# Kernel optimization log

Measured on AMD Instinct MI355X. Metric: run time of the kernel, lower is better.

Reference implementation:

```python
import jax, jax.numpy as jnp
import numpy as np

D_MODEL = 1024
N_SA = 8          # self-attention heads
N_RA = 8          # relational-attention heads
TOTAL = N_SA + N_RA
HEAD_DIM = D_MODEL // TOTAL   # 64
KEY_DIM = HEAD_DIM            # default key_dim = d_model // total_n_heads
N_REL = 8                     # n_relations (= n_heads_ra default)
REL_PROJ = KEY_DIM            # rel_proj_dim default
B, S = 4, 1024


def _rope(x, cos, sin):
    # x: [b, s, h, d]; cos/sin: [s, d//2]; interleaved-pair rotation as in apply_rotary_emb
    xr = x.reshape(x.shape[:-1] + (-1, 2))
    x_r, x_i = xr[..., 0], xr[..., 1]
    c = cos[None, :, None, :]
    s = sin[None, :, None, :]
    o_r = x_r * c - x_i * s
    o_i = x_r * s + x_i * c
    return jnp.stack([o_r, o_i], axis=-1).reshape(x.shape)


def setup_inputs() -> dict:
    key = jax.random.key(0)
    ks = jax.random.split(key, 16)
    def p(k, shape, scale=0.02):
        return jax.random.normal(k, shape, dtype=jnp.float32) * scale
    x = jax.random.normal(ks[0], (B, S, D_MODEL), dtype=jnp.float32)
    symbols = jax.random.normal(ks[1], (B, S, D_MODEL), dtype=jnp.float32)
    # standard RoPE frequency tables, shape [S, KEY_DIM//2]
    inv_freq = 1.0 / (10000.0 ** (np.arange(0, KEY_DIM, 2, dtype=np.float32) / KEY_DIM))
    ang = np.outer(np.arange(S, dtype=np.float32), inv_freq)
    freqs_cos = jnp.asarray(np.cos(ang), dtype=jnp.float32)
    freqs_sin = jnp.asarray(np.sin(ang), dtype=jnp.float32)
    return dict(
        x=x, symbols=symbols, freqs_cos=freqs_cos, freqs_sin=freqs_sin,
        # self-attention stream params
        wq_sa=p(ks[2], (D_MODEL, N_SA * KEY_DIM)),
        wk_sa=p(ks[3], (D_MODEL, N_SA * KEY_DIM)),
        wv_sa=p(ks[4], (D_MODEL, N_SA * HEAD_DIM)),
        wo_sa=p(ks[5], (N_SA * HEAD_DIM, N_SA * HEAD_DIM)),
        # relational-attention stream params
        wq_attn=p(ks[6], (D_MODEL, N_RA * KEY_DIM)),
        wk_attn=p(ks[7], (D_MODEL, N_RA * KEY_DIM)),
        wq_rel=p(ks[8], (D_MODEL, N_REL * REL_PROJ)),
        wk_rel=p(ks[9], (D_MODEL, N_REL * REL_PROJ)),
        wr=p(ks[10], (N_RA, HEAD_DIM, N_REL)),      # per-head relation->head_dim map
        wv_sym=p(ks[11], (D_MODEL, N_RA * HEAD_DIM)),  # symbol projection
        wo_ra=p(ks[12], (N_RA * HEAD_DIM, N_RA * HEAD_DIM)),
    )


def reference(x, symbols, freqs_cos, freqs_sin, wq_sa, wk_sa, wv_sa, wo_sa,
              wq_attn, wk_attn, wq_rel, wk_rel, wr, wv_sym, wo_ra):
    b, s, _ = x.shape
    attn_scale = 1.0 / jnp.sqrt(jnp.asarray(HEAD_DIM, dtype=x.dtype))
    rel_scale = 1.0 / jnp.sqrt(jnp.asarray(REL_PROJ, dtype=x.dtype))
    causal = jnp.tril(jnp.ones((s, s), dtype=bool))
    neg = jnp.where(causal, jnp.asarray(0.0, x.dtype), jnp.asarray(-jnp.inf, x.dtype))

    # ---- standard self-attention stream ----
    q = _rope((x @ wq_sa).reshape(b, s, N_SA, KEY_DIM), freqs_cos, freqs_sin)
    k = _rope((x @ wk_sa).reshape(b, s, N_SA, KEY_DIM), freqs_cos, freqs_sin)
    v = (x @ wv_sa).reshape(b, s, N_SA, HEAD_DIM)
    scores = jnp.einsum('bihd,bjhd->bhij', q, k) * attn_scale + neg
    attn = jax.nn.softmax(scores, axis=-1)
    sa_out = jnp.einsum('bhij,bjhd->bihd', attn, v).reshape(b, s, -1) @ wo_sa

    # ---- relational attention stream ----
    qa = _rope((x @ wq_attn).reshape(b, s, N_RA, KEY_DIM), freqs_cos, freqs_sin)
    ka = _rope((x @ wk_attn).reshape(b, s, N_RA, KEY_DIM), freqs_cos, freqs_sin)
    ra_scores = jnp.einsum('bihd,bjhd->bhij', qa, ka) * attn_scale + neg
    ra_attn = jax.nn.softmax(ra_scores, axis=-1)
    # relations r(i,j) in R^{n_rel}: inner products of relation projections, tanh-activated
    qr = (x @ wq_rel).reshape(b, s, N_REL, REL_PROJ)
    kr = (x @ wk_rel).reshape(b, s, N_REL, REL_PROJ)
    rel = jnp.tanh(jnp.einsum('bird,bjrd->bijr', qr, kr) * rel_scale)  # [b,s,s,n_rel]
    sv = (symbols @ wv_sym).reshape(b, s, N_RA, HEAD_DIM)
    sym_msg = jnp.einsum('bhij,bjhd->bihd', ra_attn, sv)
    rel_msg = jnp.einsum('bhij,bijr->bihr', ra_attn, rel)
    rel_proj = jnp.einsum('bihr,hdr->bihd', rel_msg, wr)
    ra_out = (sym_msg + rel_proj).reshape(b, s, -1) @ wo_ra

    # dual attention: concat the two streams along feature dim -> [b, s, d_model]
    return jnp.concatenate([sa_out, ra_out], axis=-1)
```

## Files before the change

kernel.cpp:

```cpp
#include <hip/hip_runtime.h>

typedef unsigned short u16;
typedef unsigned int u32;
typedef __attribute__((ext_vector_type(8))) short s16x8;
typedef __attribute__((ext_vector_type(4))) float f32x4;

#define C_QSA 0
#define C_KSA 512
#define C_VSA 1024
#define C_QA  1536
#define C_KA  2048
#define C_QR  2560
#define C_KR  3072
#define C_SV  3584
#define LDP   4096

__device__ __forceinline__ u16 f2bf(float f) {
    union { float f; unsigned u; } v; v.f = f;
    return (u16)((v.u + 0x7FFFu + ((v.u >> 16) & 1u)) >> 16);
}
__device__ __forceinline__ float bf2f(u16 h) {
    union { unsigned u; float f; } v; v.u = ((unsigned)h) << 16; return v.f;
}
__device__ __forceinline__ float fexp(float y) {
    return __builtin_exp2f(y * 1.4426950408889634f);
}
__device__ __forceinline__ float ftanh(float x) {
    float e = __builtin_exp2f(x * 2.885390081777927f);
    return 1.f - 2.f / (e + 1.f);
}
__device__ __forceinline__ f32x4 mfma16(s16x8 a, s16x8 b, f32x4 c) {
    return __builtin_amdgcn_mfma_f32_16x16x32_bf16(a, b, c, 0, 0, 0);
}
__device__ __forceinline__ void gload16(const u16* g, u16* l) {
    __builtin_amdgcn_global_load_lds(
        (const __attribute__((address_space(1))) void*)g,
        (__attribute__((address_space(3))) void*)l, 16, 0, 0);
}


__global__ void cvt2_f32_bf16(const float* __restrict__ a, const float* __restrict__ b,
                              u16* __restrict__ oa, u16* __restrict__ ob) {
    int i = (blockIdx.x * 256 + threadIdx.x) * 8;
    const int half = (i >= 4194304) ? 1 : 0;
    const float* in = half ? b : a;
    u16* out = half ? ob : oa;
    int off = i - half * 4194304;
    float4 x = *(const float4*)(in + off);
    float4 y = *(const float4*)(in + off + 4);
    s16x8 o;
    o[0] = (short)f2bf(x.x); o[1] = (short)f2bf(x.y);
    o[2] = (short)f2bf(x.z); o[3] = (short)f2bf(x.w);
    o[4] = (short)f2bf(y.x); o[5] = (short)f2bf(y.y);
    o[6] = (short)f2bf(y.z); o[7] = (short)f2bf(y.w);
    *(s16x8*)(out + off) = o;
}

struct WP { const float* p[10]; };

__global__ void transpose_w(WP wp, u16* __restrict__ WcatT,
                            u16* __restrict__ woSaT, u16* __restrict__ woRaT) {
    const int z = blockIdx.z;
    const float* W;
    u16* Wt;
    int K;
    if (z < 8) { W = wp.p[z]; Wt = WcatT + (size_t)z * 524288; K = 1024; }
    else       { W = wp.p[z]; Wt = (z == 8) ? woSaT : woRaT;   K = 512;  }
    const int N = 512;
    const int kt = blockIdx.x * 32, nt = blockIdx.y * 32;
    if (kt >= K) return;
    __shared__ float t[32][33];
    const int c = threadIdx.x & 31, r0 = threadIdx.x >> 5;
#pragma unroll
    for (int it = 0; it < 4; ++it) {
        int r = it * 8 + r0;
        t[r][c] = W[(size_t)(kt + r) * N + nt + c];
    }
    __syncthreads();
#pragma unroll
    for (int it = 0; it < 4; ++it) {
        int r = it * 8 + r0;
        Wt[(size_t)(nt + r) * K + kt + c] = f2bf(t[c][r]);
    }
}

__global__ void transpose_v2(const u16* __restrict__ P, u16* __restrict__ Vt, int colOff) {
    const int st = blockIdx.x * 32, ht = blockIdx.y * 32, b = blockIdx.z;
    __shared__ u16 t[32][34];
    const int c = threadIdx.x & 31, r0 = threadIdx.x >> 5;
#pragma unroll
    for (int it = 0; it < 4; ++it) {
        int r = it * 8 + r0;
        t[r][c] = P[(size_t)(b * 1024 + st + r) * LDP + colOff + ht + c];
    }
    __syncthreads();
    const int cp = ((c & 15) >> 2) * 8 + (c >> 4) * 4 + (c & 3);
#pragma unroll
    for (int it = 0; it < 4; ++it) {
        int r = it * 8 + r0;
        Vt[(size_t)b * 524288 + (size_t)(ht + r) * 1024 + st + cp] = t[c][r];
    }
}


__global__ void rope_kernel(u16* __restrict__ P, const float* __restrict__ fcos,
                            const float* __restrict__ fsin) {
    int idx = blockIdx.x * 256 + threadIdx.x;
    int row = idx >> 10;
    int rem = idx & 1023;
    int region = rem >> 8;
    int pr = rem & 255;
    int head = pr >> 5, p = pr & 31;
    int off = (region + (region >> 1)) * 512;
    int col = off + head * 64 + 2 * p;
    int s = row & 1023;
    float c = fcos[s * 32 + p], sn = fsin[s * 32 + p];
    u32* ptr = (u32*)(P + (size_t)row * LDP + col);
    u32 v = *ptr;
    float xr = bf2f((u16)(v & 0xffff)), xi = bf2f((u16)(v >> 16));
    u16 o0 = f2bf(xr * c - xi * sn);
    u16 o1 = f2bf(xr * sn + xi * c);
    *ptr = (u32)o0 | ((u32)o1 << 16);
}


template<bool OUT_BF16, bool SWZ>
__global__ __launch_bounds__(256) void gemm_bf16(
    const u16* __restrict__ A, const u16* __restrict__ A2, int lda, int nswitch,
    const u16* __restrict__ Bt, int ldb,
    void* __restrict__ Cp, int ldc, int ccolOff, int K)
{
    __shared__ u16 As[128][64];
    __shared__ u16 Bs[128][64];
    const int tid = threadIdx.x;
    int bx = blockIdx.x, by = blockIdx.y;
    if (SWZ) {
        int lin = by * gridDim.x + bx;
        int k = lin & 7, j = lin >> 3;
        bx = (k & 3) * 8 + (j & 7);
        by = (k >> 2) * 16 + (j >> 3);
    }
    const int m0 = bx * 128, n0 = by * 128;
    const u16* Ause = (A2 != nullptr && n0 >= nswitch) ? A2 : A;
    const int w = tid >> 6, lane = tid & 63;
    const int w32 = w * 32;
    const int wm = (w >> 1) * 64, wn = (w & 1) * 64;
    const int lr = lane & 15, lg = lane >> 4;
    const int srow = lane >> 3;
    const int sc16 = ((lane & 7) ^ srow) * 8;
    f32x4 acc[4][4] = {};

    for (int k0 = 0; k0 < K; k0 += 64) {
        const u16* ga = &Ause[(size_t)(m0 + w32 + srow) * lda + k0 + sc16];
        const u16* gb = &Bt [(size_t)(n0 + w32 + srow) * ldb + k0 + sc16];
        gload16(ga,            &As[w32][0]);
        gload16(ga +  8 * lda, &As[w32 +  8][0]);
        gload16(ga + 16 * lda, &As[w32 + 16][0]);
        gload16(ga + 24 * lda, &As[w32 + 24][0]);
        gload16(gb,            &Bs[w32][0]);
        gload16(gb +  8 * ldb, &Bs[w32 +  8][0]);
        gload16(gb + 16 * ldb, &Bs[w32 + 16][0]);
        gload16(gb + 24 * ldb, &Bs[w32 + 24][0]);
        __syncthreads();
#pragma unroll
        for (int kk = 0; kk < 2; ++kk) {
            s16x8 af[4], bfr[4];
#pragma unroll
            for (int t = 0; t < 4; ++t) {
                const int ca = (((kk * 4 + lg) ^ (lr & 7)) * 8);
                af[t]  = *(const s16x8*)&As[wm + t * 16 + lr][ca];
                bfr[t] = *(const s16x8*)&Bs[wn + t * 16 + lr][ca];
            }
#pragma unroll
            for (int i = 0; i < 4; ++i)
#pragma unroll
                for (int j = 0; j < 4; ++j)
                    acc[i][j] = mfma16(af[i], bfr[j], acc[i][j]);
        }
        __syncthreads();
    }
#pragma unroll
    for (int i = 0; i < 4; ++i)
#pragma unroll
        for (int j = 0; j < 4; ++j)
#pragma unroll
            for (int r = 0; r < 4; ++r) {
                int row = m0 + wm + i * 16 + lg * 4 + r;
                int col = n0 + wn + j * 16 + lr;
                float val = acc[i][j][r];
                if (OUT_BF16)
                    ((u16*)Cp)[(size_t)row * ldc + ccolOff + col] = f2bf(val);
                else
                    ((float*)Cp)[(size_t)row * ldc + ccolOff + col] = val;
            }
}


__global__ __launch_bounds__(64) void attn_sa(u16* __restrict__ P, const u16* __restrict__ Vt) {
    const int bid = blockIdx.x;
    const int h = bid & 7;
    const int b = (bid >> 3) & 3;
    const int pr = bid >> 5;
    const int xt1 = pr, xt2 = 63 - pr;
    const int lane = threadIdx.x, lr = lane & 15, lg = lane >> 4;
    const size_t rowBase = (size_t)b * 1024;
    const int i0_1 = xt1 * 16, i0_2 = xt2 * 16;
    const int ir1 = i0_1 + lr, ir2 = i0_2 + lr;

    const u16* Kbase = P + rowBase * LDP + (C_KSA + h * 64);
    const u16* Vb = Vt + ((size_t)(b * 8 + h)) * 65536;

    s16x8 q1[2], q2[2];
    {
        const u16* q = P + (rowBase + ir1) * LDP + (C_QSA + h * 64) + lg * 8;
        q1[0] = *(const s16x8*)q; q1[1] = *(const s16x8*)(q + 32);
        q = P + (rowBase + ir2) * LDP + (C_QSA + h * 64) + lg * 8;
        q2[0] = *(const s16x8*)q; q2[1] = *(const s16x8*)(q + 32);
    }
    f32x4 o1[4] = {}, o2[4] = {};
    float l1 = 0.f, l2 = 0.f;
    const int njt  = (xt2 >> 1) + 1;
    const int njt1 = (xt1 >> 1) + 1;

    for (int jt = 0; jt < njt; ++jt) {
        const int j0 = jt * 32;
        const bool act1 = (jt < njt1);
        s16x8 kf[2][2], vfr[4];
#pragma unroll
        for (int sub = 0; sub < 2; ++sub) {
            const u16* kp = Kbase + (size_t)(j0 + sub * 16 + lr) * LDP + lg * 8;
            kf[sub][0] = *(const s16x8*)kp;
            kf[sub][1] = *(const s16x8*)(kp + 32);
        }
#pragma unroll
        for (int ds = 0; ds < 4; ++ds)
            vfr[ds] = *(const s16x8*)(Vb + (size_t)(ds * 16 + lr) * 1024 + j0 + 8 * lg);

        f32x4 sc2[2] = {{0.f,0.f,0.f,0.f},{0.f,0.f,0.f,0.f}};
        f32x4 sc1[2] = {{0.f,0.f,0.f,0.f},{0.f,0.f,0.f,0.f}};
#pragma unroll
        for (int sub = 0; sub < 2; ++sub) {
            sc2[sub] = mfma16(kf[sub][0], q2[0], sc2[sub]);
            sc2[sub] = mfma16(kf[sub][1], q2[1], sc2[sub]);
        }
        if (act1) {
#pragma unroll
            for (int sub = 0; sub < 2; ++sub) {
                sc1[sub] = mfma16(kf[sub][0], q1[0], sc1[sub]);
                sc1[sub] = mfma16(kf[sub][1], q1[1], sc1[sub]);
            }
        }
        s16x8 pa;
#pragma unroll
        for (int sub = 0; sub < 2; ++sub)
#pragma unroll
            for (int r = 0; r < 4; ++r) {
                int j = j0 + sub * 16 + 4 * lg + r;
                float p = (j <= ir2) ? fexp(sc2[sub][r] * 0.125f) : 0.f;
                l2 += p;
                pa[sub * 4 + r] = (short)f2bf(p);
            }
#pragma unroll
        for (int ds = 0; ds < 4; ++ds) o2[ds] = mfma16(pa, vfr[ds], o2[ds]);
        if (act1) {
#pragma unroll
            for (int sub = 0; sub < 2; ++sub)
#pragma unroll
                for (int r = 0; r < 4; ++r) {
                    int j = j0 + sub * 16 + 4 * lg + r;
                    float p = (j <= ir1) ? fexp(sc1[sub][r] * 0.125f) : 0.f;
                    l1 += p;
                    pa[sub * 4 + r] = (short)f2bf(p);
                }
#pragma unroll
            for (int ds = 0; ds < 4; ++ds) o1[ds] = mfma16(pa, vfr[ds], o1[ds]);
        }
    }
    l1 += __shfl_xor(l1, 16); l1 += __shfl_xor(l1, 32);
    l2 += __shfl_xor(l2, 16); l2 += __shfl_xor(l2, 32);
    float li1[4], li2[4];
#pragma unroll
    for (int r = 0; r < 4; ++r) {
        li1[r] = 1.f / __shfl(l1, 4 * lg + r);
        li2[r] = 1.f / __shfl(l2, 4 * lg + r);
    }
#pragma unroll
    for (int ds = 0; ds < 4; ++ds)
#pragma unroll
        for (int r = 0; r < 4; ++r) {
            P[(rowBase + i0_1 + 4 * lg + r) * LDP + (C_QSA + h * 64) + ds * 16 + lr] =
                f2bf(o1[ds][r] * li1[r]);
            P[(rowBase + i0_2 + 4 * lg + r) * LDP + (C_QSA + h * 64) + ds * 16 + lr] =
                f2bf(o2[ds][r] * li2[r]);
        }
}


__global__ __launch_bounds__(512) void attn_ra(u16* __restrict__ P, const u16* __restrict__ SVt,
                                               float* __restrict__ opart,
                                               float* __restrict__ mlr) {
    const int bid = blockIdx.x;
    const int slot = bid & 7;
    const int b = slot & 3, s = slot >> 2;
    const int xt = 63 - (bid >> 3);
    const int w = threadIdx.x >> 6, lane = threadIdx.x & 63;
    const int lr = lane & 15, lg = lane >> 4;
    const int h = w;
    const size_t rowBase = (size_t)b * 1024;
    const int i0 = xt * 16;
    const int ir = i0 + lr;

    __shared__ float relT[2][2][32][16][8];

    const u16* Kbase  = P + rowBase * LDP + (C_KA + h * 64);
    const u16* KRbase = P + rowBase * LDP + (C_KR + h * 64);
    const u16* Vb = SVt + ((size_t)(b * 8 + h)) * 65536;

    s16x8 qf[2], qrf[2];
    {
        const u16* q = P + (rowBase + ir) * LDP + (C_QA + h * 64) + lg * 8;
        qf[0] = *(const s16x8*)q; qf[1] = *(const s16x8*)(q + 32);
        const u16* qr = P + (rowBase + ir) * LDP + (C_QR + h * 64) + lg * 8;
        qrf[0] = *(const s16x8*)qr; qrf[1] = *(const s16x8*)(qr + 32);
    }
    f32x4 o[4] = {};
    float rmr[8] = {};
    float l = 0.f;
    const int njt = (xt >> 1) + 1;
    const int cnt = (njt - s + 1) >> 1;
    const int npair = (cnt + 1) >> 1;
    const int slotw = (w + lr) & 7;

    for (int u = 0; u < npair; ++u) {
        const int j0a = (s + 4 * u) * 32;
        const bool actB = (2 * u + 1) < cnt;
        const int j0b = actB ? j0a + 64 : j0a;
        s16x8 kfA[2][2], krA[2][2], kfB[2][2], krB[2][2], vfA[4], vfB[4];
#pragma unroll
        for (int sub = 0; sub < 2; ++sub) {
            const u16* kp = Kbase + (size_t)(j0a + sub * 16 + lr) * LDP + lg * 8;
            kfA[sub][0] = *(const s16x8*)kp;  kfA[sub][1] = *(const s16x8*)(kp + 32);
            const u16* krp = KRbase + (size_t)(j0a + sub * 16 + lr) * LDP + lg * 8;
            krA[sub][0] = *(const s16x8*)krp; krA[sub][1] = *(const s16x8*)(krp + 32);
            kp = Kbase + (size_t)(j0b + sub * 16 + lr) * LDP + lg * 8;
            kfB[sub][0] = *(const s16x8*)kp;  kfB[sub][1] = *(const s16x8*)(kp + 32);
            krp = KRbase + (size_t)(j0b + sub * 16 + lr) * LDP + lg * 8;
            krB[sub][0] = *(const s16x8*)krp; krB[sub][1] = *(const s16x8*)(krp + 32);
        }
#pragma unroll
        for (int ds = 0; ds < 4; ++ds) {
            vfA[ds] = *(const s16x8*)(Vb + (size_t)(ds * 16 + lr) * 1024 + j0a + 8 * lg);
            vfB[ds] = *(const s16x8*)(Vb + (size_t)(ds * 16 + lr) * 1024 + j0b + 8 * lg);
        }
        f32x4 scA[2] = {{0.f,0.f,0.f,0.f},{0.f,0.f,0.f,0.f}};
        f32x4 scB[2] = {{0.f,0.f,0.f,0.f},{0.f,0.f,0.f,0.f}};
        f32x4 rtA[2] = {{0.f,0.f,0.f,0.f},{0.f,0.f,0.f,0.f}};
        f32x4 rtB[2] = {{0.f,0.f,0.f,0.f},{0.f,0.f,0.f,0.f}};
#pragma unroll
        for (int sub = 0; sub < 2; ++sub) {
            scA[sub] = mfma16(kfA[sub][0], qf[0], scA[sub]);
            scA[sub] = mfma16(kfA[sub][1], qf[1], scA[sub]);
            rtA[sub] = mfma16(krA[sub][0], qrf[0], rtA[sub]);
            rtA[sub] = mfma16(krA[sub][1], qrf[1], rtA[sub]);
            scB[sub] = mfma16(kfB[sub][0], qf[0], scB[sub]);
            scB[sub] = mfma16(kfB[sub][1], qf[1], scB[sub]);
            rtB[sub] = mfma16(krB[sub][0], qrf[0], rtB[sub]);
            rtB[sub] = mfma16(krB[sub][1], qrf[1], rtB[sub]);
        }
        float pA[2][4], pB[2][4];
#pragma unroll
        for (int sub = 0; sub < 2; ++sub)
#pragma unroll
            for (int r = 0; r < 4; ++r) {
                int jA = j0a + sub * 16 + 4 * lg + r;
                int jB = j0b + sub * 16 + 4 * lg + r;
                pA[sub][r] = (jA <= ir) ? fexp(scA[sub][r] * 0.125f) : 0.f;
                pB[sub][r] = (actB && jB <= ir) ? fexp(scB[sub][r] * 0.125f) : 0.f;
                l += pA[sub][r] + pB[sub][r];
            }
#pragma unroll
        for (int sub = 0; sub < 2; ++sub)
#pragma unroll
            for (int r = 0; r < 4; ++r) {
                int jp = sub * 16 + 4 * lg + r;
                relT[u & 1][0][jp][lr][slotw] = ftanh(rtA[sub][r] * 0.125f);
                relT[u & 1][1][jp][lr][slotw] = ftanh(rtB[sub][r] * 0.125f);
            }
        __syncthreads();
#pragma unroll
        for (int sub = 0; sub < 2; ++sub)
#pragma unroll
            for (int r = 0; r < 4; ++r) {
                int jp = sub * 16 + 4 * lg + r;
                f32x4 a  = *(const f32x4*)&relT[u & 1][0][jp][lr][0];
                f32x4 bb = *(const f32x4*)&relT[u & 1][0][jp][lr][4];
                float pv = pA[sub][r];
#pragma unroll
                for (int k = 0; k < 4; ++k) {
                    rmr[k]     += pv * a[k];
                    rmr[4 + k] += pv * bb[k];
                }
                a  = *(const f32x4*)&relT[u & 1][1][jp][lr][0];
                bb = *(const f32x4*)&relT[u & 1][1][jp][lr][4];
                pv = pB[sub][r];
#pragma unroll
                for (int k = 0; k < 4; ++k) {
                    rmr[k]     += pv * a[k];
                    rmr[4 + k] += pv * bb[k];
                }
            }
        s16x8 paA, paB;
#pragma unroll
        for (int r = 0; r < 4; ++r) {
            paA[r]     = (short)f2bf(pA[0][r]);
            paA[4 + r] = (short)f2bf(pA[1][r]);
            paB[r]     = (short)f2bf(pB[0][r]);
            paB[4 + r] = (short)f2bf(pB[1][r]);
        }
#pragma unroll
        for (int ds = 0; ds < 4; ++ds) {
            o[ds] = mfma16(paA, vfA[ds], o[ds]);
            o[ds] = mfma16(paB, vfB[ds], o[ds]);
        }
    }

    l += __shfl_xor(l, 16); l += __shfl_xor(l, 32);
#pragma unroll
    for (int k = 0; k < 8; ++k) {
        float v = rmr[k];
        v += __shfl_xor(v, 16);
        v += __shfl_xor(v, 32);
        rmr[k] = v;
    }
    float g[8], t0[8];
    const int t = lr & 7;
#pragma unroll
    for (int k = 0; k < 8; ++k) g[k] = rmr[k];
#pragma unroll
    for (int k = 0; k < 8; ++k) t0[k] = (t & 1) ? g[(k + 1) & 7] : g[k];
#pragma unroll
    for (int k = 0; k < 8; ++k) g[k]  = (t & 2) ? t0[(k + 2) & 7] : t0[k];
#pragma unroll
    for (int k = 0; k < 8; ++k) t0[k] = (t & 4) ? g[(k + 4) & 7] : g[k];

    const int headRow = (b * 8 + h) * 1024;
#pragma unroll
    for (int ds = 0; ds < 4; ++ds)
#pragma unroll
        for (int r = 0; r < 4; ++r) {
            int row = headRow + i0 + 4 * lg + r;
            opart[((size_t)row * 2 + s) * 64 + ds * 16 + lr] = o[ds][r];
        }
    if (lg == 0) {
        float* pm = &mlr[((size_t)(headRow + i0 + lr) * 2 + s) * 10];
        pm[0] = l;
#pragma unroll
        for (int c = 0; c < 8; ++c) pm[1 + c] = t0[c];
    }
}


__global__ __launch_bounds__(256) void merge_ra(const float* __restrict__ opart,
                                                const float* __restrict__ mlr,
                                                const float* __restrict__ wr,
                                                u16* __restrict__ P) {
    const int gid = blockIdx.x * 4 + (threadIdx.x >> 6);
    const int d = threadIdx.x & 63;
    const int i = gid & 1023;
    const int h = (gid >> 10) & 7;
    const int b = gid >> 13;
    const float* ml0 = &mlr[(size_t)gid * 20];
    const float* ml1 = ml0 + 10;
    float ilt = 1.f / (ml0[0] + ml1[0]);
    float acc = (opart[(size_t)gid * 128 + d] +
                 opart[(size_t)gid * 128 + 64 + d]) * ilt;
#pragma unroll
    for (int c = 0; c < 8; ++c) {
        float rm = (ml0[1 + c] + ml1[1 + c]) * ilt;
        acc += rm * wr[h * 512 + d * 8 + c];
    }
    P[((size_t)(b * 1024 + i)) * LDP + C_QA + h * 64 + d] = f2bf(acc);
}


extern "C" void kernel_launch(void* const* d_in, const int* in_sizes, int n_in,
                              void* d_out, int out_size, void* d_ws, size_t ws_size,
                              hipStream_t stream)
{
    const float* x     = (const float*)d_in[0];
    const float* sym   = (const float*)d_in[1];
    const float* fcos  = (const float*)d_in[2];
    const float* fsin  = (const float*)d_in[3];
    const float* w_qsa = (const float*)d_in[4];
    const float* w_ksa = (const float*)d_in[5];
    const float* w_vsa = (const float*)d_in[6];
    const float* w_osa = (const float*)d_in[7];
    const float* w_qa  = (const float*)d_in[8];
    const float* w_ka  = (const float*)d_in[9];
    const float* w_qr  = (const float*)d_in[10];
    const float* w_kr  = (const float*)d_in[11];
    const float* wr    = (const float*)d_in[12];
    const float* w_sv  = (const float*)d_in[13];
    const float* w_ora = (const float*)d_in[14];

    char* ws = (char*)d_ws;
    u16* xb    = (u16*)(ws);
    u16* symb  = (u16*)(ws + (8u  << 20));
    u16* WcatT = (u16*)(ws + (16u << 20));
    u16* woSaT = (u16*)(ws + (24u << 20));
    u16* woRaT = (u16*)(ws + (24u << 20) + (512u << 10));
    u16* Pcat  = (u16*)(ws + (25u << 20));
    u16* vT    = (u16*)(ws + (57u << 20));
    u16* svT   = (u16*)(ws + (61u << 20));
    float* opart = (float*)(ws);
    float* mlrp  = (float*)(ws + (17u << 20));

    cvt2_f32_bf16<<<4096, 256, 0, stream>>>(x, sym, xb, symb);

    WP wp{{w_qsa, w_ksa, w_vsa, w_qa, w_ka, w_qr, w_kr, w_sv, w_osa, w_ora}};
    transpose_w<<<dim3(32, 16, 10), 256, 0, stream>>>(wp, WcatT, woSaT, woRaT);

    gemm_bf16<true, true><<<dim3(32, 32), 256, 0, stream>>>(
        xb, symb, 1024, C_SV, WcatT, 1024, Pcat, LDP, 0, 1024);

    rope_kernel<<<16384, 256, 0, stream>>>(Pcat, fcos, fsin);

    transpose_v2<<<dim3(32, 16, 4), 256, 0, stream>>>(Pcat, vT,  C_VSA);
    transpose_v2<<<dim3(32, 16, 4), 256, 0, stream>>>(Pcat, svT, C_SV);

    attn_sa<<<1024, 64, 0, stream>>>(Pcat, vT);
    attn_ra<<<512, 512, 0, stream>>>(Pcat, svT, opart, mlrp);
    merge_ra<<<8192, 256, 0, stream>>>(opart, mlrp, wr, Pcat);

    gemm_bf16<false, false><<<dim3(32, 8), 256, 0, stream>>>(
        Pcat + C_QSA, Pcat + C_QA, LDP, 512, woSaT, 512, d_out, 1024, 0, 512);
}
```

Measured before the change: 202.5 us.

## Fuse self-attention and relational-attention kernels into one interleaved launch

Merges the separate self-attention and relational-attention kernels into a single 768-block launch in which every third block row does self-attention (8 waves, one per head, on a 16-row tile) and the rest do relational attention. The aim is to remove a launch boundary and let the cheaper self-attention work fill gaps beside the heavier relational blocks. The self-attention path drops its earlier pairing of short and long causal tiles in favour of per-head waves with descending tile order. The relational path now uses a single-buffered shared relation tile with an extra barrier per iteration, which adds synchronisation in exchange for half the shared memory.

```diff
diff --git a/kernel.cpp b/kernel.cpp
--- a/kernel.cpp
+++ b/kernel.cpp
@@ -196,121 +196,91 @@
 }
 
 
-__global__ __launch_bounds__(64) void attn_sa(u16* __restrict__ P, const u16* __restrict__ Vt) {
+__global__ __launch_bounds__(512) void attn_fused(
+    u16* __restrict__ P, const u16* __restrict__ Vt, const u16* __restrict__ SVt,
+    float* __restrict__ opart, float* __restrict__ mlr)
+{
+    __shared__ float relT[2][32][16][8];
     const int bid = blockIdx.x;
-    const int h = bid & 7;
-    const int b = (bid >> 3) & 3;
-    const int pr = bid >> 5;
-    const int xt1 = pr, xt2 = 63 - pr;
-    const int lane = threadIdx.x, lr = lane & 15, lg = lane >> 4;
-    const size_t rowBase = (size_t)b * 1024;
-    const int i0_1 = xt1 * 16, i0_2 = xt2 * 16;
-    const int ir1 = i0_1 + lr, ir2 = i0_2 + lr;
-
-    const u16* Kbase = P + rowBase * LDP + (C_KSA + h * 64);
-    const u16* Vb = Vt + ((size_t)(b * 8 + h)) * 65536;
-
-    s16x8 q1[2], q2[2];
-    {
-        const u16* q = P + (rowBase + ir1) * LDP + (C_QSA + h * 64) + lg * 8;
-        q1[0] = *(const s16x8*)q; q1[1] = *(const s16x8*)(q + 32);
-        q = P + (rowBase + ir2) * LDP + (C_QSA + h * 64) + lg * 8;
-        q2[0] = *(const s16x8*)q; q2[1] = *(const s16x8*)(q + 32);
-    }
-    f32x4 o1[4] = {}, o2[4] = {};
-    float l1 = 0.f, l2 = 0.f;
-    const int njt  = (xt2 >> 1) + 1;
-    const int njt1 = (xt1 >> 1) + 1;
-
-    for (int jt = 0; jt < njt; ++jt) {
-        const int j0 = jt * 32;
-        const bool act1 = (jt < njt1);
-        s16x8 kf[2][2], vfr[4];
-#pragma unroll
-        for (int sub = 0; sub < 2; ++sub) {
-            const u16* kp = Kbase + (size_t)(j0 + sub * 16 + lr) * LDP + lg * 8;
-            kf[sub][0] = *(const s16x8*)kp;
-            kf[sub][1] = *(const s16x8*)(kp + 32);
-        }
-#pragma unroll
-        for (int ds = 0; ds < 4; ++ds)
-            vfr[ds] = *(const s16x8*)(Vb + (size_t)(ds * 16 + lr) * 1024 + j0 + 8 * lg);
-
-        f32x4 sc2[2] = {{0.f,0.f,0.f,0.f},{0.f,0.f,0.f,0.f}};
-        f32x4 sc1[2] = {{0.f,0.f,0.f,0.f},{0.f,0.f,0.f,0.f}};
-#pragma unroll
-        for (int sub = 0; sub < 2; ++sub) {
-            sc2[sub] = mfma16(kf[sub][0], q2[0], sc2[sub]);
-            sc2[sub] = mfma16(kf[sub][1], q2[1], sc2[sub]);
-        }
-        if (act1) {
-#pragma unroll
-            for (int sub = 0; sub < 2; ++sub) {
-                sc1[sub] = mfma16(kf[sub][0], q1[0], sc1[sub]);
-                sc1[sub] = mfma16(kf[sub][1], q1[1], sc1[sub]);
-            }
-        }
-        s16x8 pa;
-#pragma unroll
-        for (int sub = 0; sub < 2; ++sub)
-#pragma unroll
-            for (int r = 0; r < 4; ++r) {
-                int j = j0 + sub * 16 + 4 * lg + r;
-                float p = (j <= ir2) ? fexp(sc2[sub][r] * 0.125f) : 0.f;
-                l2 += p;
-                pa[sub * 4 + r] = (short)f2bf(p);
-            }
-#pragma unroll
-        for (int ds = 0; ds < 4; ++ds) o2[ds] = mfma16(pa, vfr[ds], o2[ds]);
-        if (act1) {
-#pragma unroll
-            for (int sub = 0; sub < 2; ++sub)
-#pragma unroll
-                for (int r = 0; r < 4; ++r) {
-                    int j = j0 + sub * 16 + 4 * lg + r;
-                    float p = (j <= ir1) ? fexp(sc1[sub][r] * 0.125f) : 0.f;
-                    l1 += p;
-                    pa[sub * 4 + r] = (short)f2bf(p);
-                }
-#pragma unroll
-            for (int ds = 0; ds < 4; ++ds) o1[ds] = mfma16(pa, vfr[ds], o1[ds]);
-        }
-    }
-    l1 += __shfl_xor(l1, 16); l1 += __shfl_xor(l1, 32);
-    l2 += __shfl_xor(l2, 16); l2 += __shfl_xor(l2, 32);
-    float li1[4], li2[4];
-#pragma unroll
-    for (int r = 0; r < 4; ++r) {
-        li1[r] = 1.f / __shfl(l1, 4 * lg + r);
-        li2[r] = 1.f / __shfl(l2, 4 * lg + r);
-    }
-#pragma unroll
-    for (int ds = 0; ds < 4; ++ds)
-#pragma unroll
-        for (int r = 0; r < 4; ++r) {
-            P[(rowBase + i0_1 + 4 * lg + r) * LDP + (C_QSA + h * 64) + ds * 16 + lr] =
-                f2bf(o1[ds][r] * li1[r]);
-            P[(rowBase + i0_2 + 4 * lg + r) * LDP + (C_QSA + h * 64) + ds * 16 + lr] =
-                f2bf(o2[ds][r] * li2[r]);
-        }
-}
-
-
-__global__ __launch_bounds__(512) void attn_ra(u16* __restrict__ P, const u16* __restrict__ SVt,
-                                               float* __restrict__ opart,
-                                               float* __restrict__ mlr) {
-    const int bid = blockIdx.x;
-    const int slot = bid & 7;
-    const int b = slot & 3, s = slot >> 2;
-    const int xt = 63 - (bid >> 3);
+    const int r = bid >> 3, xcd = bid & 7;
     const int w = threadIdx.x >> 6, lane = threadIdx.x & 63;
     const int lr = lane & 15, lg = lane >> 4;
+    const int rm3 = r % 3;
+
+    if (rm3 == 2) {
+        const int sa_blk = (r / 3) * 8 + xcd;
+        const int h = w;
+        const int b = sa_blk & 3;
+        const int xt = 63 - (sa_blk >> 2);
+        const size_t rowBase = (size_t)b * 1024;
+        const int i0 = xt * 16;
+        const int ir = i0 + lr;
+        const u16* Kbase = P + rowBase * LDP + (C_KSA + h * 64);
+        const u16* Vb = Vt + ((size_t)(b * 8 + h)) * 65536;
+
+        s16x8 qf[2];
+        {
+            const u16* q = P + (rowBase + ir) * LDP + (C_QSA + h * 64) + lg * 8;
+            qf[0] = *(const s16x8*)q;
+            qf[1] = *(const s16x8*)(q + 32);
+        }
+        f32x4 o[4] = {};
+        float l = 0.f;
+        const int njt = (xt >> 1) + 1;
+
+        for (int jt = 0; jt < njt; ++jt) {
+            const int j0 = jt * 32;
+            s16x8 kf[2][2], vfr[4];
+#pragma unroll
+            for (int sub = 0; sub < 2; ++sub) {
+                const u16* kp = Kbase + (size_t)(j0 + sub * 16 + lr) * LDP + lg * 8;
+                kf[sub][0] = *(const s16x8*)kp;
+                kf[sub][1] = *(const s16x8*)(kp + 32);
+            }
+#pragma unroll
+            for (int ds = 0; ds < 4; ++ds)
+                vfr[ds] = *(const s16x8*)(Vb + (size_t)(ds * 16 + lr) * 1024 + j0 + 8 * lg);
+
+            f32x4 sc[2] = {{0.f,0.f,0.f,0.f},{0.f,0.f,0.f,0.f}};
+#pragma unroll
+            for (int sub = 0; sub < 2; ++sub) {
+                sc[sub] = mfma16(kf[sub][0], qf[0], sc[sub]);
+                sc[sub] = mfma16(kf[sub][1], qf[1], sc[sub]);
+            }
+            s16x8 pa;
+#pragma unroll
+            for (int sub = 0; sub < 2; ++sub)
+#pragma unroll
+                for (int rr = 0; rr < 4; ++rr) {
+                    int j = j0 + sub * 16 + 4 * lg + rr;
+                    float p = (j <= ir) ? fexp(sc[sub][rr] * 0.125f) : 0.f;
+                    l += p;
+                    pa[sub * 4 + rr] = (short)f2bf(p);
+                }
+#pragma unroll
+            for (int ds = 0; ds < 4; ++ds) o[ds] = mfma16(pa, vfr[ds], o[ds]);
+        }
+        l += __shfl_xor(l, 16); l += __shfl_xor(l, 32);
+        float li[4];
+#pragma unroll
+        for (int rr = 0; rr < 4; ++rr) li[rr] = 1.f / __shfl(l, 4 * lg + rr);
+#pragma unroll
+        for (int ds = 0; ds < 4; ++ds)
+#pragma unroll
+            for (int rr = 0; rr < 4; ++rr)
+                P[(rowBase + i0 + 4 * lg + rr) * LDP + (C_QSA + h * 64) + ds * 16 + lr] =
+                    f2bf(o[ds][rr] * li[rr]);
+        return;
+    }
+
+    const int ra_idx = ((r / 3) * 2 + rm3) * 8 + xcd;
+    const int slot = ra_idx & 7;
+    const int b = slot & 3, s = slot >> 2;
+    const int xt = 63 - (ra_idx >> 3);
     const int h = w;
     const size_t rowBase = (size_t)b * 1024;
     const int i0 = xt * 16;
     const int ir = i0 + lr;
-
-    __shared__ float relT[2][2][32][16][8];
 
     const u16* Kbase  = P + rowBase * LDP + (C_KA + h * 64);
     const u16* KRbase = P + rowBase * LDP + (C_KR + h * 64);
@@ -371,38 +341,39 @@
 #pragma unroll
         for (int sub = 0; sub < 2; ++sub)
 #pragma unroll
-            for (int r = 0; r < 4; ++r) {
-                int jA = j0a + sub * 16 + 4 * lg + r;
-                int jB = j0b + sub * 16 + 4 * lg + r;
-                pA[sub][r] = (jA <= ir) ? fexp(scA[sub][r] * 0.125f) : 0.f;
-                pB[sub][r] = (actB && jB <= ir) ? fexp(scB[sub][r] * 0.125f) : 0.f;
-                l += pA[sub][r] + pB[sub][r];
-            }
+            for (int rr = 0; rr < 4; ++rr) {
+                int jA = j0a + sub * 16 + 4 * lg + rr;
+                int jB = j0b + sub * 16 + 4 * lg + rr;
+                pA[sub][rr] = (jA <= ir) ? fexp(scA[sub][rr] * 0.125f) : 0.f;
+                pB[sub][rr] = (actB && jB <= ir) ? fexp(scB[sub][rr] * 0.125f) : 0.f;
+                l += pA[sub][rr] + pB[sub][rr];
+            }
+        __syncthreads();
 #pragma unroll
         for (int sub = 0; sub < 2; ++sub)
 #pragma unroll
-            for (int r = 0; r < 4; ++r) {
-                int jp = sub * 16 + 4 * lg + r;
-                relT[u & 1][0][jp][lr][slotw] = ftanh(rtA[sub][r] * 0.125f);
-                relT[u & 1][1][jp][lr][slotw] = ftanh(rtB[sub][r] * 0.125f);
+            for (int rr = 0; rr < 4; ++rr) {
+                int jp = sub * 16 + 4 * lg + rr;
+                relT[0][jp][lr][slotw] = ftanh(rtA[sub][rr] * 0.125f);
+                relT[1][jp][lr][slotw] = ftanh(rtB[sub][rr] * 0.125f);
             }
         __syncthreads();
 #pragma unroll
         for (int sub = 0; sub < 2; ++sub)
 #pragma unroll
-            for (int r = 0; r < 4; ++r) {
-                int jp = sub * 16 + 4 * lg + r;
-                f32x4 a  = *(const f32x4*)&relT[u & 1][0][jp][lr][0];
-                f32x4 bb = *(const f32x4*)&relT[u & 1][0][jp][lr][4];
-                float pv = pA[sub][r];
+            for (int rr = 0; rr < 4; ++rr) {
+                int jp = sub * 16 + 4 * lg + rr;
+                f32x4 a  = *(const f32x4*)&relT[0][jp][lr][0];
+                f32x4 bb = *(const f32x4*)&relT[0][jp][lr][4];
+                float pv = pA[sub][rr];
 #pragma unroll
                 for (int k = 0; k < 4; ++k) {
                     rmr[k]     += pv * a[k];
                     rmr[4 + k] += pv * bb[k];
                 }
-                a  = *(const f32x4*)&relT[u & 1][1][jp][lr][0];
-                bb = *(const f32x4*)&relT[u & 1][1][jp][lr][4];
-                pv = pB[sub][r];
+                a  = *(const f32x4*)&relT[1][jp][lr][0];
+                bb = *(const f32x4*)&relT[1][jp][lr][4];
+                pv = pB[sub][rr];
 #pragma unroll
                 for (int k = 0; k < 4; ++k) {
                     rmr[k]     += pv * a[k];
@@ -411,11 +382,11 @@
             }
         s16x8 paA, paB;
 #pragma unroll
-        for (int r = 0; r < 4; ++r) {
-            paA[r]     = (short)f2bf(pA[0][r]);
-            paA[4 + r] = (short)f2bf(pA[1][r]);
-            paB[r]     = (short)f2bf(pB[0][r]);
-            paB[4 + r] = (short)f2bf(pB[1][r]);
+        for (int rr = 0; rr < 4; ++rr) {
+            paA[rr]     = (short)f2bf(pA[0][rr]);
+            paA[4 + rr] = (short)f2bf(pA[1][rr]);
+            paB[rr]     = (short)f2bf(pB[0][rr]);
+            paB[4 + rr] = (short)f2bf(pB[1][rr]);
         }
 #pragma unroll
         for (int ds = 0; ds < 4; ++ds) {
@@ -447,9 +418,9 @@
 #pragma unroll
     for (int ds = 0; ds < 4; ++ds)
 #pragma unroll
-        for (int r = 0; r < 4; ++r) {
-            int row = headRow + i0 + 4 * lg + r;
-            opart[((size_t)row * 2 + s) * 64 + ds * 16 + lr] = o[ds][r];
+        for (int rr = 0; rr < 4; ++rr) {
+            int row = headRow + i0 + 4 * lg + rr;
+            opart[((size_t)row * 2 + s) * 64 + ds * 16 + lr] = o[ds][rr];
         }
     if (lg == 0) {
         float* pm = &mlr[((size_t)(headRow + i0 + lr) * 2 + s) * 10];
@@ -528,8 +499,7 @@
     transpose_v2<<<dim3(32, 16, 4), 256, 0, stream>>>(Pcat, vT,  C_VSA);
     transpose_v2<<<dim3(32, 16, 4), 256, 0, stream>>>(Pcat, svT, C_SV);
 
-    attn_sa<<<1024, 64, 0, stream>>>(Pcat, vT);
-    attn_ra<<<512, 512, 0, stream>>>(Pcat, svT, opart, mlrp);
+    attn_fused<<<768, 512, 0, stream>>>(Pcat, vT, svT, opart, mlrp);
     merge_ra<<<8192, 256, 0, stream>>>(opart, mlrp, wr, Pcat);
 
     gemm_bf16<false, false><<<dim3(32, 8), 256, 0, stream>>>(
```

Measured after the change: 218.4 us. 1.08x slower.

## Split relational attention KV range four ways and store partials in bf16

Applied to the files above, without the earlier changes.

The relational-attention kernel now splits each query tile's key range across four blocks instead of two, doubling the grid to 1024 blocks so more CUs have work. Partial outputs are stored as bf16 rather than fp32 to cut merge traffic, and the merge kernel sums four partials. The shared relation buffer loses its double-buffer dimension and gains an extra barrier instead. Risks: less work per block, extra merge reads, bf16 rounding of partials, and the added synchronization.

```diff
diff --git a/kernel.cpp b/kernel.cpp
--- a/kernel.cpp
+++ b/kernel.cpp
@@ -297,20 +297,21 @@
 
 
 __global__ __launch_bounds__(512) void attn_ra(u16* __restrict__ P, const u16* __restrict__ SVt,
-                                               float* __restrict__ opart,
+                                               u16* __restrict__ opart,
                                                float* __restrict__ mlr) {
     const int bid = blockIdx.x;
-    const int slot = bid & 7;
-    const int b = slot & 3, s = slot >> 2;
-    const int xt = 63 - (bid >> 3);
+    const int b = bid & 3;
+    const int s = (bid >> 2) & 3;
+    const int xt = 63 - (bid >> 4);
     const int w = threadIdx.x >> 6, lane = threadIdx.x & 63;
     const int lr = lane & 15, lg = lane >> 4;
     const int h = w;
     const size_t rowBase = (size_t)b * 1024;
     const int i0 = xt * 16;
     const int ir = i0 + lr;
-
-    __shared__ float relT[2][2][32][16][8];
+    const int slotw = (w + lr) & 7;
+
+    __shared__ float relT[2][32][16][8];
 
     const u16* Kbase  = P + rowBase * LDP + (C_KA + h * 64);
     const u16* KRbase = P + rowBase * LDP + (C_KR + h * 64);
@@ -327,14 +328,13 @@
     float rmr[8] = {};
     float l = 0.f;
     const int njt = (xt >> 1) + 1;
-    const int cnt = (njt - s + 1) >> 1;
+    const int cnt = (njt > s) ? ((njt - s + 3) >> 2) : 0;
     const int npair = (cnt + 1) >> 1;
-    const int slotw = (w + lr) & 7;
 
     for (int u = 0; u < npair; ++u) {
-        const int j0a = (s + 4 * u) * 32;
+        const int j0a = (s + 8 * u) * 32;
         const bool actB = (2 * u + 1) < cnt;
-        const int j0b = actB ? j0a + 64 : j0a;
+        const int j0b = actB ? j0a + 128 : j0a;
         s16x8 kfA[2][2], krA[2][2], kfB[2][2], krB[2][2], vfA[4], vfB[4];
 #pragma unroll
         for (int sub = 0; sub < 2; ++sub) {
@@ -378,13 +378,14 @@
                 pB[sub][r] = (actB && jB <= ir) ? fexp(scB[sub][r] * 0.125f) : 0.f;
                 l += pA[sub][r] + pB[sub][r];
             }
+        __syncthreads();
 #pragma unroll
         for (int sub = 0; sub < 2; ++sub)
 #pragma unroll
             for (int r = 0; r < 4; ++r) {
                 int jp = sub * 16 + 4 * lg + r;
-                relT[u & 1][0][jp][lr][slotw] = ftanh(rtA[sub][r] * 0.125f);
-                relT[u & 1][1][jp][lr][slotw] = ftanh(rtB[sub][r] * 0.125f);
+                relT[0][jp][lr][slotw] = ftanh(rtA[sub][r] * 0.125f);
+                relT[1][jp][lr][slotw] = ftanh(rtB[sub][r] * 0.125f);
             }
         __syncthreads();
 #pragma unroll
@@ -392,16 +393,16 @@
 #pragma unroll
             for (int r = 0; r < 4; ++r) {
                 int jp = sub * 16 + 4 * lg + r;
-                f32x4 a  = *(const f32x4*)&relT[u & 1][0][jp][lr][0];
-                f32x4 bb = *(const f32x4*)&relT[u & 1][0][jp][lr][4];
+                f32x4 a  = *(const f32x4*)&relT[0][jp][lr][0];
+                f32x4 bb = *(const f32x4*)&relT[0][jp][lr][4];
                 float pv = pA[sub][r];
 #pragma unroll
                 for (int k = 0; k < 4; ++k) {
                     rmr[k]     += pv * a[k];
                     rmr[4 + k] += pv * bb[k];
                 }
-                a  = *(const f32x4*)&relT[u & 1][1][jp][lr][0];
-                bb = *(const f32x4*)&relT[u & 1][1][jp][lr][4];
+                a  = *(const f32x4*)&relT[1][jp][lr][0];
+                bb = *(const f32x4*)&relT[1][jp][lr][4];
                 pv = pB[sub][r];
 #pragma unroll
                 for (int k = 0; k < 4; ++k) {
@@ -449,10 +450,10 @@
 #pragma unroll
         for (int r = 0; r < 4; ++r) {
             int row = headRow + i0 + 4 * lg + r;
-            opart[((size_t)row * 2 + s) * 64 + ds * 16 + lr] = o[ds][r];
+            opart[(size_t)row * 256 + s * 64 + ds * 16 + lr] = f2bf(o[ds][r]);
         }
     if (lg == 0) {
-        float* pm = &mlr[((size_t)(headRow + i0 + lr) * 2 + s) * 10];
+        float* pm = &mlr[((size_t)(headRow + i0 + lr) * 4 + s) * 9];
         pm[0] = l;
 #pragma unroll
         for (int c = 0; c < 8; ++c) pm[1 + c] = t0[c];
@@ -460,7 +461,7 @@
 }
 
 
-__global__ __launch_bounds__(256) void merge_ra(const float* __restrict__ opart,
+__global__ __launch_bounds__(256) void merge_ra(const u16* __restrict__ opart,
                                                 const float* __restrict__ mlr,
                                                 const float* __restrict__ wr,
                                                 u16* __restrict__ P) {
@@ -469,16 +470,20 @@
     const int i = gid & 1023;
     const int h = (gid >> 10) & 7;
     const int b = gid >> 13;
-    const float* ml0 = &mlr[(size_t)gid * 20];
-    const float* ml1 = ml0 + 10;
-    float ilt = 1.f / (ml0[0] + ml1[0]);
-    float acc = (opart[(size_t)gid * 128 + d] +
-                 opart[(size_t)gid * 128 + 64 + d]) * ilt;
-#pragma unroll
-    for (int c = 0; c < 8; ++c) {
-        float rm = (ml0[1 + c] + ml1[1 + c]) * ilt;
-        acc += rm * wr[h * 512 + d * 8 + c];
-    }
+    float lt = 0.f, osum = 0.f, rm[8] = {};
+#pragma unroll
+    for (int s = 0; s < 4; ++s) {
+        const float* pm = &mlr[((size_t)gid * 4 + s) * 9];
+        lt += pm[0];
+#pragma unroll
+        for (int c = 0; c < 8; ++c) rm[c] += pm[1 + c];
+        osum += bf2f(opart[(size_t)gid * 256 + s * 64 + d]);
+    }
+    float ilt = 1.f / lt;
+    float acc = osum * ilt;
+#pragma unroll
+    for (int c = 0; c < 8; ++c)
+        acc += rm[c] * ilt * wr[h * 512 + d * 8 + c];
     P[((size_t)(b * 1024 + i)) * LDP + C_QA + h * 64 + d] = f2bf(acc);
 }
 
@@ -512,7 +517,7 @@
     u16* Pcat  = (u16*)(ws + (25u << 20));
     u16* vT    = (u16*)(ws + (57u << 20));
     u16* svT   = (u16*)(ws + (61u << 20));
-    float* opart = (float*)(ws);
+    u16*   opart = (u16*)(ws);
     float* mlrp  = (float*)(ws + (17u << 20));
 
     cvt2_f32_bf16<<<4096, 256, 0, stream>>>(x, sym, xb, symb);
@@ -529,7 +534,7 @@
     transpose_v2<<<dim3(32, 16, 4), 256, 0, stream>>>(Pcat, svT, C_SV);
 
     attn_sa<<<1024, 64, 0, stream>>>(Pcat, vT);
-    attn_ra<<<512, 512, 0, stream>>>(Pcat, svT, opart, mlrp);
+    attn_ra<<<1024, 512, 0, stream>>>(Pcat, svT, opart, mlrp);
     merge_ra<<<8192, 256, 0, stream>>>(opart, mlrp, wr, Pcat);
 
     gemm_bf16<false, false><<<dim3(32, 8), 256, 0, stream>>>(
```

Measured after the change: 223.9 us. 10.6% more time.

## Split self-attention key loop across four waves with LDS reduction

Applied to the files above, without the earlier changes.

The self-attention kernel now launches 256 threads per block, and the four waves stride over key tiles instead of one wave walking them all. Each wave writes its partial output accumulators and row sums to shared memory. After a barrier, two waves sum the partials, normalise and store the result. This is meant to cut the per-block serial latency of the causal key loop and raise the number of waves in flight. In exchange it adds 36KB of LDS per block, a barrier and a reduction pass, which may limit how many blocks stay resident.

```diff
diff --git a/kernel.cpp b/kernel.cpp
--- a/kernel.cpp
+++ b/kernel.cpp
@@ -196,16 +196,20 @@
 }
 
 
-__global__ __launch_bounds__(64) void attn_sa(u16* __restrict__ P, const u16* __restrict__ Vt) {
+__global__ __launch_bounds__(256) void attn_sa(u16* __restrict__ P, const u16* __restrict__ Vt) {
     const int bid = blockIdx.x;
     const int h = bid & 7;
     const int b = (bid >> 3) & 3;
     const int pr = bid >> 5;
+    const int w = threadIdx.x >> 6, lane = threadIdx.x & 63;
+    const int lr = lane & 15, lg = lane >> 4;
+    const size_t rowBase = (size_t)b * 1024;
     const int xt1 = pr, xt2 = 63 - pr;
-    const int lane = threadIdx.x, lr = lane & 15, lg = lane >> 4;
-    const size_t rowBase = (size_t)b * 1024;
     const int i0_1 = xt1 * 16, i0_2 = xt2 * 16;
     const int ir1 = i0_1 + lr, ir2 = i0_2 + lr;
+
+    __shared__ float oL[4][2][16][64];
+    __shared__ float lL[4][2][64];
 
     const u16* Kbase = P + rowBase * LDP + (C_KSA + h * 64);
     const u16* Vb = Vt + ((size_t)(b * 8 + h)) * 65536;
@@ -222,7 +226,7 @@
     const int njt  = (xt2 >> 1) + 1;
     const int njt1 = (xt1 >> 1) + 1;
 
-    for (int jt = 0; jt < njt; ++jt) {
+    for (int jt = w; jt < njt; jt += 4) {
         const int j0 = jt * 32;
         const bool act1 = (jt < njt1);
         s16x8 kf[2][2], vfr[4];
@@ -276,23 +280,42 @@
             for (int ds = 0; ds < 4; ++ds) o1[ds] = mfma16(pa, vfr[ds], o1[ds]);
         }
     }
-    l1 += __shfl_xor(l1, 16); l1 += __shfl_xor(l1, 32);
-    l2 += __shfl_xor(l2, 16); l2 += __shfl_xor(l2, 32);
-    float li1[4], li2[4];
-#pragma unroll
-    for (int r = 0; r < 4; ++r) {
-        li1[r] = 1.f / __shfl(l1, 4 * lg + r);
-        li2[r] = 1.f / __shfl(l2, 4 * lg + r);
-    }
 #pragma unroll
     for (int ds = 0; ds < 4; ++ds)
 #pragma unroll
         for (int r = 0; r < 4; ++r) {
-            P[(rowBase + i0_1 + 4 * lg + r) * LDP + (C_QSA + h * 64) + ds * 16 + lr] =
-                f2bf(o1[ds][r] * li1[r]);
-            P[(rowBase + i0_2 + 4 * lg + r) * LDP + (C_QSA + h * 64) + ds * 16 + lr] =
-                f2bf(o2[ds][r] * li2[r]);
-        }
+            oL[w][0][ds * 4 + r][lane] = o1[ds][r];
+            oL[w][1][ds * 4 + r][lane] = o2[ds][r];
+        }
+    lL[w][0][lane] = l1;
+    lL[w][1][lane] = l2;
+    __syncthreads();
+    if (w < 2) {
+        const int i0 = w ? i0_2 : i0_1;
+        f32x4 o[4];
+        float l = 0.f;
+#pragma unroll
+        for (int v = 0; v < 4; ++v) l += lL[v][w][lane];
+#pragma unroll
+        for (int ds = 0; ds < 4; ++ds)
+#pragma unroll
+            for (int r = 0; r < 4; ++r) {
+                float acc = 0.f;
+#pragma unroll
+                for (int v = 0; v < 4; ++v) acc += oL[v][w][ds * 4 + r][lane];
+                o[ds][r] = acc;
+            }
+        l += __shfl_xor(l, 16); l += __shfl_xor(l, 32);
+        float li[4];
+#pragma unroll
+        for (int r = 0; r < 4; ++r) li[r] = 1.f / __shfl(l, 4 * lg + r);
+#pragma unroll
+        for (int ds = 0; ds < 4; ++ds)
+#pragma unroll
+            for (int r = 0; r < 4; ++r)
+                P[(rowBase + i0 + 4 * lg + r) * LDP + (C_QSA + h * 64) + ds * 16 + lr] =
+                    f2bf(o[ds][r] * li[r]);
+    }
 }
 
 
@@ -528,7 +551,7 @@
     transpose_v2<<<dim3(32, 16, 4), 256, 0, stream>>>(Pcat, vT,  C_VSA);
     transpose_v2<<<dim3(32, 16, 4), 256, 0, stream>>>(Pcat, svT, C_SV);
 
-    attn_sa<<<1024, 64, 0, stream>>>(Pcat, vT);
+    attn_sa<<<1024, 256, 0, stream>>>(Pcat, vT);
     attn_ra<<<512, 512, 0, stream>>>(Pcat, svT, opart, mlrp);
     merge_ra<<<8192, 256, 0, stream>>>(opart, mlrp, wr, Pcat);
 
```

After: 204.5 us. Within noise of the previous version (+0.9%).
